# Kernel optimization log

Hardware: AMD Instinct MI355X
Metric: run time of the kernel (lower is better)

The kernel has to match this reference:

```python
import jax, jax.numpy as jnp
import numpy as np

N = 50000      # nodes
DEG = 32       # avg degree
E = N * DEG + N  # edges incl. self loops
IN_DIM = 512
H = 4          # heads
D = 128        # hidden per head
SLOPE = 0.2


def setup_inputs() -> dict:
    key = jax.random.key(0)
    ks = jax.random.split(key, 12)
    features = jax.random.normal(ks[0], (N, IN_DIM), dtype=jnp.float32)
    src_r = jax.random.randint(ks[1], (N * DEG,), 0, N)
    dst_r = jax.random.randint(ks[2], (N * DEG,), 0, N)
    loop = jnp.arange(N)
    src = jnp.concatenate([src_r, loop]).astype(jnp.int32)
    dst = jnp.concatenate([dst_r, loop]).astype(jnp.int32)
    ids = jax.random.randint(ks[3], (16,), 0, N)
    s0 = 1.0 / np.sqrt(IN_DIM)
    s1 = 1.0 / np.sqrt(H * D)
    fc_w0 = jax.random.normal(ks[4], (IN_DIM, H * D), dtype=jnp.float32) * s0
    attn_l0 = jax.random.normal(ks[5], (H, D), dtype=jnp.float32) * s1
    attn_r0 = jax.random.normal(ks[6], (H, D), dtype=jnp.float32) * s1
    bias0 = jnp.zeros((H * D,), dtype=jnp.float32)
    fc_w1 = jax.random.normal(ks[7], (H * D, H * D), dtype=jnp.float32) * s1
    attn_l1 = jax.random.normal(ks[8], (H, D), dtype=jnp.float32) * s1
    attn_r1 = jax.random.normal(ks[9], (H, D), dtype=jnp.float32) * s1
    bias1 = jnp.zeros((H * D,), dtype=jnp.float32)
    return dict(features=features, fc_w0=fc_w0, attn_l0=attn_l0, attn_r0=attn_r0,
                bias0=bias0, fc_w1=fc_w1, attn_l1=attn_l1, attn_r1=attn_r1,
                bias1=bias1, src=src, dst=dst, ids=ids)


def gat_layer(h, fc_w, attn_l, attn_r, bias, src, dst, residual):
    ft = (h @ fc_w).reshape(N, H, D)                     # [N,H,D]
    el = jnp.sum(ft * attn_l, axis=-1)                   # [N,H]
    er = jnp.sum(ft * attn_r, axis=-1)                   # [N,H]
    e = jax.nn.leaky_relu(el[src] + er[dst], SLOPE)      # [E,H]
    # edge softmax over incoming edges of each dst node (self-loops guarantee coverage)
    emax = jax.ops.segment_max(e, dst, num_segments=N)   # [N,H]
    ee = jnp.exp(e - emax[dst])
    esum = jax.ops.segment_sum(ee, dst, num_segments=N)  # [N,H]
    alpha = ee / esum[dst]                               # [E,H]
    out = jax.ops.segment_sum(alpha[:, :, None] * ft[src], dst, num_segments=N)  # [N,H,D]
    if residual:
        out = out + h.reshape(N, H, D)                   # res_fc is Identity (in == H*D)
    out = out + bias.reshape(1, H, D)
    out = jax.nn.elu(out)
    return out.reshape(N, H * D)


def reference(features, fc_w0, attn_l0, attn_r0, bias0, fc_w1, attn_l1, attn_r1,
              bias1, src, dst, ids):
    h = gat_layer(features, fc_w0, attn_l0, attn_r0, bias0, src, dst, residual=False)
    h = gat_layer(h, fc_w1, attn_l1, attn_r1, bias1, src, dst, residual=True)
    h = jnp.tanh(h)
    return h[ids]  # [B, H*D] gather per id2node lookup
```

## Files before the change

kernel.cpp:

```cpp
#include <hip/hip_runtime.h>
#include <hip/hip_bf16.h>

typedef short bf16x8 __attribute__((ext_vector_type(8)));
typedef float f32x4 __attribute__((ext_vector_type(4)));

#define HD 512
#define KDIM 512
#define NHEAD 4
#define DHEAD 128
#define C1CAP 1024
#define C2CAP 16384
#define E1CAP 2048
#define E2CAP 32768

__global__ void detect_k(const unsigned short* __restrict__ feat, int* __restrict__ flagp) {
    __shared__ int cs;
    if (threadIdx.x == 0) cs = 0;
    __syncthreads();
    int c = 0;
    for (int k = 0; k < 16; ++k) {
        unsigned short u = feat[2 * (threadIdx.x + k * 256)];
        int e = (u >> 7) & 0xFF;
        if (e >= 96 && e <= 140) c++;
    }
    atomicAdd(&cs, c);
    __syncthreads();
    if (threadIdx.x == 0) *flagp = (cs > 2048) ? 1 : 0;
}

__global__ __launch_bounds__(256) void prep_k(
    const void* __restrict__ W0, const void* __restrict__ W1,
    __hip_bfloat16* __restrict__ Wt0, __hip_bfloat16* __restrict__ Wt1,
    const void* p0, const void* p1, const void* p2,
    const void* p3, const void* p4, const void* p5,
    float* __restrict__ smallc,
    const int* __restrict__ ids, int B,
    int* __restrict__ mapId, unsigned* __restrict__ bmId,
    const int* __restrict__ flagp) {
    const int isbf = *flagp;
    const int b = blockIdx.x;
    const int t = threadIdx.x;
    if (b < 2048) {
        const void* W = (b < 1024) ? W0 : W1;
        __hip_bfloat16* Wt = (b < 1024) ? Wt0 : Wt1;
        int idx = ((b < 1024) ? b : b - 1024) * 256 + t;
        int i = idx >> 9;
        int j = idx & 511;
        float v = isbf ? __bfloat162float(((const __hip_bfloat16*)W)[idx])
                       : ((const float*)W)[idx];
        Wt[j * 512 + i] = __float2bfloat16(v);
    } else if (b < 2054) {
        int which = b - 2048;
        const void* p;
        switch (which) {
            case 0: p = p0; break;
            case 1: p = p1; break;
            case 2: p = p2; break;
            case 3: p = p3; break;
            case 4: p = p4; break;
            default: p = p5; break;
        }
#pragma unroll
        for (int r = 0; r < 2; ++r) {
            int e = t + r * 256;
            float v = isbf ? __bfloat162float(((const __hip_bfloat16*)p)[e])
                           : ((const float*)p)[e];
            smallc[which * 512 + e] = v;
        }
    } else {
        if (t < B) {
            int n = ids[t];
            mapId[n] = t;
            atomicOr(&bmId[n >> 5], 1u << (n & 31));
        }
    }
}

__global__ __launch_bounds__(256) void scan_k(
    const int* __restrict__ dst, int E,
    const unsigned* __restrict__ bm,
    unsigned long long* __restrict__ masks) {
    const int gid = blockIdx.x * 256 + threadIdx.x;
    const bool inb = (4 * gid < E);
    int4 d4 = {0, 0, 0, 0};
    if (inb) d4 = ((const int4*)dst)[gid];
    const int dv[4] = {d4.x, d4.y, d4.z, d4.w};
    unsigned long long m[4];
#pragma unroll
    for (int k = 0; k < 4; ++k) {
        int d = dv[k];
        bool hit = inb && ((bm[d >> 5] >> (d & 31)) & 1u);
        m[k] = __ballot(hit);
    }
    const int w = gid >> 6, lane = gid & 63;
    if (lane < 4) {
        unsigned long long v = (lane == 0) ? m[0] : (lane == 1) ? m[1]
                             : (lane == 2) ? m[2] : m[3];
        masks[(size_t)w * 4 + lane] = v;
    }
}

__global__ __launch_bounds__(256) void emit_k(
    const unsigned long long* __restrict__ masks, int nmask,
    const int* __restrict__ src, const int* __restrict__ dst,
    const int* __restrict__ mapd,
    int2* __restrict__ elist, int* __restrict__ ecnt, int cap,
    int* __restrict__ mapm, int* __restrict__ Flist,
    int* __restrict__ nF, int fcap, unsigned* __restrict__ bmOut) {
    int j = blockIdx.x * 256 + threadIdx.x;
    if (j >= nmask) return;
    unsigned long long m = masks[j];
    if (!m) return;
    const int w = j >> 2, k = j & 3;
    while (m) {
        int l = __ffsll((long long)m) - 1;
        m &= m - 1;
        int e = w * 256 + l * 4 + k;
        int s = src[e], d = dst[e];
        int p = atomicAdd(ecnt, 1);
        if (p < cap) { int2 v; v.x = s; v.y = mapd[d]; elist[p] = v; }
        if (atomicCAS(&mapm[s], -1, -2) == -1) {
            int q = atomicAdd(nF, 1);
            if (q < fcap) { Flist[q] = s; mapm[s] = q; }
            else mapm[s] = 0;
            if (bmOut) atomicOr(&bmOut[s >> 5], 1u << (s & 31));
        }
    }
}

__global__ __launch_bounds__(1024) void csr_k(
    const int2* __restrict__ E1, const int* __restrict__ nE1p,
    const int2* __restrict__ E2, const int* __restrict__ nE2p,
    const int* __restrict__ map1, const int* __restrict__ map2,
    int* __restrict__ off1, int* __restrict__ off2,
    int* __restrict__ b1, int* __restrict__ b2) {
    __shared__ int cnt[1024];
    __shared__ int scn[1024];
    __shared__ int cur[1024];
    __shared__ int c1[16];
    __shared__ int o1cur[16];
    const int t = threadIdx.x;
    int n1 = *nE1p; if (n1 > E1CAP) n1 = E1CAP;
    int n2 = *nE2p; if (n2 > E2CAP) n2 = E2CAP;
    cnt[t] = 0;
    if (t < 16) c1[t] = 0;
    __syncthreads();
    for (int i = t; i < n2; i += 1024) atomicAdd(&cnt[E2[i].y], 1);
    for (int i = t; i < n1; i += 1024) atomicAdd(&c1[E1[i].y], 1);
    __syncthreads();
    int v = cnt[t];
    scn[t] = v;
    __syncthreads();
    for (int off = 1; off < 1024; off <<= 1) {
        int x = (t >= off) ? scn[t - off] : 0;
        __syncthreads();
        scn[t] += x;
        __syncthreads();
    }
    int ex = scn[t] - v;
    off2[t] = ex;
    cur[t] = ex;
    if (t == 1023) off2[1024] = scn[1023];
    if (t == 0) {
        int a = 0;
        for (int i = 0; i < 16; ++i) { off1[i] = a; o1cur[i] = a; a += c1[i]; }
        off1[16] = a;
    }
    __syncthreads();
    for (int i = t; i < n2; i += 1024) {
        int p = atomicAdd(&cur[E2[i].y], 1);
        int r = map2[E2[i].x]; if (r < 0) r = 0;
        b2[p] = r;
    }
    for (int i = t; i < n1; i += 1024) {
        int p = atomicAdd(&o1cur[E1[i].y], 1);
        int r = map1[E1[i].x]; if (r < 0) r = 0;
        b1[p] = r;
    }
}

__global__ __launch_bounds__(256) void gatherA_k(const void* __restrict__ feat,
                                                 const int* __restrict__ F2list,
                                                 const int* __restrict__ nF2,
                                                 __hip_bfloat16* __restrict__ Ac,
                                                 const int* __restrict__ flagp) {
    int cnt = *nF2; if (cnt > C2CAP) cnt = C2CAP;
    const int isbf = *flagp;
    const int t = threadIdx.x;
    for (int b = blockIdx.x; b < cnt; b += gridDim.x) {
        int row = F2list[b];
        __hip_bfloat162 v;
        if (isbf) {
            v = *(const __hip_bfloat162*)&((const __hip_bfloat16*)feat)[(size_t)row * KDIM + t * 2];
        } else {
            const float2 f = *(const float2*)&((const float*)feat)[(size_t)row * KDIM + t * 2];
            v.x = __float2bfloat16(f.x);
            v.y = __float2bfloat16(f.y);
        }
        *(__hip_bfloat162*)&Ac[(size_t)b * KDIM + t * 2] = v;
    }
}

__global__ __launch_bounds__(256) void gemm_c(
    const __hip_bfloat16* __restrict__ A,
    const __hip_bfloat16* __restrict__ Bt,
    __hip_bfloat16* __restrict__ C,
    const int* __restrict__ countp) {
    const int cntv = *countp;
    const int m0 = blockIdx.y * 128;
    if (m0 >= cntv) return;
    __shared__ alignas(16) __hip_bfloat16 As[128][40];
    __shared__ alignas(16) __hip_bfloat16 Bs[128][40];
    const int t = threadIdx.x;
    const int n0 = blockIdx.x * 128;
    const int lane = t & 63, wave = t >> 6;
    const int wm = (wave >> 1) * 64, wn = (wave & 1) * 64;
    const int fr = lane & 15, fk = (lane >> 4) * 8;
    const int r0 = t >> 2;
    const int c0 = (t & 3) * 8;

    int arow[2];
#pragma unroll
    for (int r = 0; r < 2; ++r) {
        int rr = m0 + r * 64 + r0;
        if (rr >= cntv) rr = cntv - 1;
        arow[r] = rr;
    }

    f32x4 acc[4][4];
#pragma unroll
    for (int i = 0; i < 4; ++i)
#pragma unroll
        for (int j = 0; j < 4; ++j)
#pragma unroll
            for (int r = 0; r < 4; ++r) acc[i][j][r] = 0.f;

    for (int kt = 0; kt < KDIM; kt += 32) {
#pragma unroll
        for (int r = 0; r < 2; ++r) {
            int row = r * 64 + r0;
            uint4 va = *(const uint4*)&A[(size_t)arow[r] * KDIM + kt + c0];
            *(uint4*)&As[row][c0] = va;
            uint4 vb = *(const uint4*)&Bt[(size_t)(n0 + row) * KDIM + kt + c0];
            *(uint4*)&Bs[row][c0] = vb;
        }
        __syncthreads();
        bf16x8 af[4], bfr[4];
#pragma unroll
        for (int i = 0; i < 4; ++i) af[i]  = *(const bf16x8*)&As[wm + i * 16 + fr][fk];
#pragma unroll
        for (int j = 0; j < 4; ++j) bfr[j] = *(const bf16x8*)&Bs[wn + j * 16 + fr][fk];
#pragma unroll
        for (int i = 0; i < 4; ++i)
#pragma unroll
            for (int j = 0; j < 4; ++j)
                acc[i][j] = __builtin_amdgcn_mfma_f32_16x16x32_bf16(af[i], bfr[j], acc[i][j], 0, 0, 0);
        __syncthreads();
    }

    const int cr = (lane >> 4) * 4;
    const int cc = lane & 15;
#pragma unroll
    for (int i = 0; i < 4; ++i)
#pragma unroll
        for (int j = 0; j < 4; ++j)
#pragma unroll
            for (int rg = 0; rg < 4; ++rg) {
                int m = m0 + wm + i * 16 + cr + rg;
                int n = n0 + wn + j * 16 + cc;
                C[(size_t)m * HD + n] = __float2bfloat16(acc[i][j][rg]);
            }
}

__global__ __launch_bounds__(256) void elc_k(const __hip_bfloat16* __restrict__ ft,
                                             const float* __restrict__ attn_l,
                                             const float* __restrict__ attn_r,
                                             const int* __restrict__ countp,
                                             float* __restrict__ el, float* __restrict__ er) {
    int cnt = *countp; if (cnt > C2CAP) cnt = C2CAP;
    const int h = threadIdx.x >> 6, lane = threadIdx.x & 63;
    const float2 al = *(const float2*)&attn_l[h * DHEAD + lane * 2];
    const float2 ar = *(const float2*)&attn_r[h * DHEAD + lane * 2];
    for (int b = blockIdx.x; b < cnt; b += gridDim.x) {
        const __hip_bfloat162 f = *(const __hip_bfloat162*)&ft[(size_t)b * HD + h * DHEAD + lane * 2];
        float fx = __bfloat162float(f.x), fy = __bfloat162float(f.y);
        float pl = fx * al.x + fy * al.y;
        float pr = fx * ar.x + fy * ar.y;
        for (int off = 32; off; off >>= 1) {
            pl += __shfl_xor(pl, off, 64);
            pr += __shfl_xor(pr, off, 64);
        }
        if (lane == 0) {
            el[b * NHEAD + h] = pl;
            er[b * NHEAD + h] = pr;
        }
    }
}

__global__ __launch_bounds__(256) void agg1_k(
    const int* __restrict__ off2, const int* __restrict__ b2,
    const int* __restrict__ F1list, const int* __restrict__ map2,
    const int* __restrict__ nF1,
    const float* __restrict__ el, const float* __restrict__ er,
    const __hip_bfloat16* __restrict__ ftc,
    const float* __restrict__ bias,
    __hip_bfloat16* __restrict__ outc) {
    int b = blockIdx.x;
    if (b >= *nF1) return;
    int n = F1list[b];
    int h = threadIdx.x >> 6, lane = threadIdx.x & 63;
    int rn = map2[n]; if (rn < 0) rn = 0;
    float ern = er[rn * NHEAD + h];
    int beg = off2[b], end = off2[b + 1];
    float m = -3.0e38f, l = 0.f, a0 = 0.f, a1 = 0.f;
    for (int i = beg; i < end; ++i) {
        int r2 = b2[i];
        float e = el[r2 * NHEAD + h] + ern;
        e = (e >= 0.f) ? e : 0.2f * e;
        float mn = fmaxf(m, e);
        float sc = __expf(m - mn);
        float w  = __expf(e - mn);
        const __hip_bfloat162 f = *(const __hip_bfloat162*)&ftc[(size_t)r2 * HD + h * DHEAD + lane * 2];
        l  = l * sc + w;
        a0 = a0 * sc + w * __bfloat162float(f.x);
        a1 = a1 * sc + w * __bfloat162float(f.y);
        m = mn;
    }
    float inv = (l > 0.f) ? 1.0f / l : 0.f;
    float o0 = a0 * inv, o1 = a1 * inv;
    const float2 bb = *(const float2*)&bias[h * DHEAD + lane * 2];
    o0 += bb.x;
    o1 += bb.y;
    o0 = (o0 > 0.f) ? o0 : expm1f(o0);
    o1 = (o1 > 0.f) ? o1 : expm1f(o1);
    __hip_bfloat162 o2;
    o2.x = __float2bfloat16(o0);
    o2.y = __float2bfloat16(o1);
    *(__hip_bfloat162*)&outc[(size_t)b * HD + h * DHEAD + lane * 2] = o2;
}

__global__ __launch_bounds__(256) void agg2_k(
    const int* __restrict__ off1, const int* __restrict__ b1,
    const int* __restrict__ ids, const int* __restrict__ mapId,
    const int* __restrict__ map1,
    const float* __restrict__ el, const float* __restrict__ er,
    const __hip_bfloat16* __restrict__ ftc,
    const __hip_bfloat16* __restrict__ resc,
    const float* __restrict__ bias,
    void* __restrict__ out, const int* __restrict__ flagp) {
    int b = blockIdx.x;
    int n = ids[b];
    int slot = mapId[n]; if (slot < 0) slot = 0;
    int h = threadIdx.x >> 6, lane = threadIdx.x & 63;
    int rn = map1[n]; if (rn < 0) rn = 0;
    float ern = er[rn * NHEAD + h];
    int beg = off1[slot], end = off1[slot + 1];
    float m = -3.0e38f, l = 0.f, a0 = 0.f, a1 = 0.f;
    for (int i = beg; i < end; ++i) {
        int r1 = b1[i];
        float e = el[r1 * NHEAD + h] + ern;
        e = (e >= 0.f) ? e : 0.2f * e;
        float mn = fmaxf(m, e);
        float sc = __expf(m - mn);
        float w  = __expf(e - mn);
        const __hip_bfloat162 f = *(const __hip_bfloat162*)&ftc[(size_t)r1 * HD + h * DHEAD + lane * 2];
        l  = l * sc + w;
        a0 = a0 * sc + w * __bfloat162float(f.x);
        a1 = a1 * sc + w * __bfloat162float(f.y);
        m = mn;
    }
    float inv = (l > 0.f) ? 1.0f / l : 0.f;
    float o0 = a0 * inv, o1 = a1 * inv;
    const __hip_bfloat162 r2v = *(const __hip_bfloat162*)&resc[(size_t)rn * HD + h * DHEAD + lane * 2];
    o0 += __bfloat162float(r2v.x);
    o1 += __bfloat162float(r2v.y);
    const float2 bb = *(const float2*)&bias[h * DHEAD + lane * 2];
    o0 += bb.x;
    o1 += bb.y;
    o0 = (o0 > 0.f) ? o0 : expm1f(o0);
    o1 = (o1 > 0.f) ? o1 : expm1f(o1);
    o0 = tanhf(o0);
    o1 = tanhf(o1);
    size_t oi = (size_t)b * HD + h * DHEAD + lane * 2;
    if (*flagp) {
        __hip_bfloat162 o2;
        o2.x = __float2bfloat16(o0);
        o2.y = __float2bfloat16(o1);
        *(__hip_bfloat162*)&((__hip_bfloat16*)out)[oi] = o2;
    } else {
        float2 o2; o2.x = o0; o2.y = o1;
        *(float2*)&((float*)out)[oi] = o2;
    }
}

extern "C" void kernel_launch(void* const* d_in, const int* in_sizes, int n_in,
                              void* d_out, int out_size, void* d_ws, size_t ws_size,
                              hipStream_t stream) {
    const void* features = d_in[0];
    const void* fc_w0    = d_in[1];
    const void* attn_l0  = d_in[2];
    const void* attn_r0  = d_in[3];
    const void* bias0    = d_in[4];
    const void* fc_w1    = d_in[5];
    const void* attn_l1  = d_in[6];
    const void* attn_r1  = d_in[7];
    const void* bias1    = d_in[8];
    const int* src = (const int*)d_in[9];
    const int* dst = (const int*)d_in[10];
    const int* ids = (const int*)d_in[11];

    const int N = in_sizes[0] / KDIM;
    const int E = in_sizes[9];
    const int B = in_sizes[11];
    const int words = (N + 31) / 32;

    const int nblk_scan = (E + 1023) / 1024;
    const int nwaves    = nblk_scan * 4;
    const int nmask     = nwaves * 4;

    char* w = (char*)d_ws;
    auto alloc = [&](size_t bytes) {
        void* p = (void*)w;
        w += (bytes + 255) & ~(size_t)255;
        return p;
    };
    __hip_bfloat16* Wt0 = (__hip_bfloat16*)alloc(512 * 512 * 2);
    __hip_bfloat16* Wt1 = (__hip_bfloat16*)alloc(512 * 512 * 2);
    float* smallc = (float*)alloc(6 * 512 * 4);
    int* maps    = (int*)alloc((size_t)3 * N * 4);
    int* mapId = maps;
    int* map1  = maps + N;
    int* map2  = maps + 2 * N;
    unsigned long long* masks = (unsigned long long*)alloc((size_t)nmask * 8);
    int2* E1l  = (int2*)alloc((size_t)E1CAP * 8);
    int2* E2l  = (int2*)alloc((size_t)E2CAP * 8);
    int* F1list = (int*)alloc(C1CAP * 4);
    int* F2list = (int*)alloc(C2CAP * 4);
    const int zwords = 8 + 2 * words;
    int* zmem   = (int*)alloc((size_t)zwords * 4);
    int* counters = zmem;
    unsigned* bmId = (unsigned*)(zmem + 8);
    unsigned* bm1  = bmId + words;
    int* off1 = (int*)alloc(17 * 4);
    int* off2 = (int*)alloc(1025 * 4);
    int* b1   = (int*)alloc(E1CAP * 4);
    int* b2   = (int*)alloc(E2CAP * 4);
    __hip_bfloat16* Ac   = (__hip_bfloat16*)alloc((size_t)C2CAP * KDIM * 2);
    __hip_bfloat16* ft0c = (__hip_bfloat16*)alloc((size_t)C2CAP * HD * 2);
    float* el0 = (float*)alloc((size_t)C2CAP * NHEAD * 4);
    float* er0 = (float*)alloc((size_t)C2CAP * NHEAD * 4);
    __hip_bfloat16* h1c  = (__hip_bfloat16*)alloc((size_t)C1CAP * HD * 2);
    __hip_bfloat16* ft1c = (__hip_bfloat16*)alloc((size_t)C1CAP * HD * 2);
    float* el1 = (float*)alloc((size_t)C1CAP * NHEAD * 4);
    float* er1 = (float*)alloc((size_t)C1CAP * NHEAD * 4);

    int* nE1  = counters + 0;
    int* nE2  = counters + 1;
    int* nF1  = counters + 2;
    int* nF2  = counters + 3;
    int* flag = counters + 4;

    hipMemsetAsync(maps, 0xFF, (size_t)3 * N * 4, stream);
    hipMemsetAsync(zmem, 0, (size_t)zwords * 4, stream);

    detect_k<<<1, 256, 0, stream>>>((const unsigned short*)features, flag);
    prep_k<<<2055, 256, 0, stream>>>(fc_w0, fc_w1, Wt0, Wt1,
                                     attn_l0, attn_r0, bias0, attn_l1, attn_r1, bias1,
                                     smallc, ids, B, mapId, bmId, flag);
    float* al0c = smallc + 0 * 512;
    float* ar0c = smallc + 1 * 512;
    float* b0c  = smallc + 2 * 512;
    float* al1c = smallc + 3 * 512;
    float* ar1c = smallc + 4 * 512;
    float* b1c  = smallc + 5 * 512;

    scan_k<<<nblk_scan, 256, 0, stream>>>(dst, E, bmId, masks);
    emit_k<<<(nmask + 255) / 256, 256, 0, stream>>>(masks, nmask, src, dst, mapId,
                                                    E1l, nE1, E1CAP,
                                                    map1, F1list, nF1, C1CAP, bm1);
    scan_k<<<nblk_scan, 256, 0, stream>>>(dst, E, bm1, masks);
    emit_k<<<(nmask + 255) / 256, 256, 0, stream>>>(masks, nmask, src, dst, map1,
                                                    E2l, nE2, E2CAP,
                                                    map2, F2list, nF2, C2CAP, nullptr);

    csr_k<<<1, 1024, 0, stream>>>(E1l, nE1, E2l, nE2, map1, map2, off1, off2, b1, b2);

    gatherA_k<<<512, 256, 0, stream>>>(features, F2list, nF2, Ac, flag);
    gemm_c<<<dim3(HD / 128, C2CAP / 128), 256, 0, stream>>>(Ac, Wt0, ft0c, nF2);
    elc_k<<<512, 256, 0, stream>>>(ft0c, al0c, ar0c, nF2, el0, er0);
    agg1_k<<<C1CAP, 256, 0, stream>>>(off2, b2, F1list, map2, nF1,
                                      el0, er0, ft0c, b0c, h1c);

    gemm_c<<<dim3(HD / 128, C1CAP / 128), 256, 0, stream>>>(h1c, Wt1, ft1c, nF1);
    elc_k<<<512, 256, 0, stream>>>(ft1c, al1c, ar1c, nF1, el1, er1);
    agg2_k<<<B, 256, 0, stream>>>(off1, b1, ids, mapId, map1,
                                  el1, er1, ft1c, h1c, b1c,
                                  d_out, flag);
}
```

Before: 374.2 us.

## Fuse pipeline into two persistent kernels with software grid barriers

Replaces the chain of about a dozen small kernel launches with two persistent 512-block kernels that move from phase to phase through a global atomic-counter barrier. The BFS frontier scan and emit passes merge into one pass that buffers edges and frontier nodes in shared memory and reserves global slots in bulk, and it also counts CSR degrees as it goes. The aim is to remove launch gaps and the masks round trip. The cost is that the spin barrier assumes all 512 blocks are resident at once, which is not guaranteed without a cooperative launch, and the GEMM and aggregation phases now run at a fixed grid size.

Result: slower. 1.024 ms (+173.7%).

```diff
diff --git a/kernel.cpp b/kernel.cpp
--- a/kernel.cpp
+++ b/kernel.cpp
@@ -12,207 +12,103 @@
 #define C2CAP 16384
 #define E1CAP 2048
 #define E2CAP 32768
-
-__global__ void detect_k(const unsigned short* __restrict__ feat, int* __restrict__ flagp) {
-    __shared__ int cs;
-    if (threadIdx.x == 0) cs = 0;
-    __syncthreads();
+#define GA 512
+
+__device__ __forceinline__ void gbar(int* cnt, int& gen) {
+    __syncthreads();
+    if (threadIdx.x == 0) {
+        __threadfence();
+        atomicAdd(cnt, 1);
+        gen += GA;
+        while (__hip_atomic_load(cnt, __ATOMIC_ACQUIRE, __HIP_MEMORY_SCOPE_AGENT) < gen)
+            __builtin_amdgcn_s_sleep(2);
+    }
+    __syncthreads();
+}
+
+__device__ int detect_bf16(const unsigned short* f) {
     int c = 0;
-    for (int k = 0; k < 16; ++k) {
-        unsigned short u = feat[2 * (threadIdx.x + k * 256)];
+#pragma unroll
+    for (int k = 0; k < 4; ++k) {
+        unsigned short u = f[2 * (threadIdx.x + k * 256)];
         int e = (u >> 7) & 0xFF;
-        if (e >= 96 && e <= 140) c++;
-    }
-    atomicAdd(&cs, c);
-    __syncthreads();
-    if (threadIdx.x == 0) *flagp = (cs > 2048) ? 1 : 0;
-}
-
-__global__ __launch_bounds__(256) void prep_k(
-    const void* __restrict__ W0, const void* __restrict__ W1,
-    __hip_bfloat16* __restrict__ Wt0, __hip_bfloat16* __restrict__ Wt1,
-    const void* p0, const void* p1, const void* p2,
-    const void* p3, const void* p4, const void* p5,
-    float* __restrict__ smallc,
-    const int* __restrict__ ids, int B,
-    int* __restrict__ mapId, unsigned* __restrict__ bmId,
-    const int* __restrict__ flagp) {
-    const int isbf = *flagp;
-    const int b = blockIdx.x;
+        c += (e >= 96 && e <= 140) ? 1 : 0;
+    }
+#pragma unroll
+    for (int off = 32; off; off >>= 1) c += __shfl_xor(c, off, 64);
+    __shared__ int s_c;
+    if (threadIdx.x == 0) s_c = 0;
+    __syncthreads();
+    if ((threadIdx.x & 63) == 0) atomicAdd(&s_c, c);
+    __syncthreads();
+    return s_c > 512;
+}
+
+__device__ void bfs_pass(const int* __restrict__ src, const int* __restrict__ dst, int E,
+                         const unsigned* __restrict__ bmIn, const int* __restrict__ mapd,
+                         int2* __restrict__ elist, int* ecnt, int ecap,
+                         int* __restrict__ cntArr,
+                         int* __restrict__ mapm, int* __restrict__ Flist, int* nFr, int fcap,
+                         unsigned* bmOut) {
+    __shared__ int2 eBuf[256];
+    __shared__ int fBuf[256];
+    __shared__ int eCnt_s, fCnt_s, eBase_s, fBase_s;
     const int t = threadIdx.x;
-    if (b < 2048) {
-        const void* W = (b < 1024) ? W0 : W1;
-        __hip_bfloat16* Wt = (b < 1024) ? Wt0 : Wt1;
-        int idx = ((b < 1024) ? b : b - 1024) * 256 + t;
-        int i = idx >> 9;
-        int j = idx & 511;
-        float v = isbf ? __bfloat162float(((const __hip_bfloat16*)W)[idx])
-                       : ((const float*)W)[idx];
-        Wt[j * 512 + i] = __float2bfloat16(v);
-    } else if (b < 2054) {
-        int which = b - 2048;
-        const void* p;
-        switch (which) {
-            case 0: p = p0; break;
-            case 1: p = p1; break;
-            case 2: p = p2; break;
-            case 3: p = p3; break;
-            case 4: p = p4; break;
-            default: p = p5; break;
-        }
-#pragma unroll
-        for (int r = 0; r < 2; ++r) {
-            int e = t + r * 256;
-            float v = isbf ? __bfloat162float(((const __hip_bfloat16*)p)[e])
-                           : ((const float*)p)[e];
-            smallc[which * 512 + e] = v;
-        }
-    } else {
-        if (t < B) {
-            int n = ids[t];
-            mapId[n] = t;
-            atomicOr(&bmId[n >> 5], 1u << (n & 31));
-        }
-    }
-}
-
-__global__ __launch_bounds__(256) void scan_k(
-    const int* __restrict__ dst, int E,
-    const unsigned* __restrict__ bm,
-    unsigned long long* __restrict__ masks) {
-    const int gid = blockIdx.x * 256 + threadIdx.x;
-    const bool inb = (4 * gid < E);
-    int4 d4 = {0, 0, 0, 0};
-    if (inb) d4 = ((const int4*)dst)[gid];
-    const int dv[4] = {d4.x, d4.y, d4.z, d4.w};
-    unsigned long long m[4];
-#pragma unroll
-    for (int k = 0; k < 4; ++k) {
-        int d = dv[k];
-        bool hit = inb && ((bm[d >> 5] >> (d & 31)) & 1u);
-        m[k] = __ballot(hit);
-    }
-    const int w = gid >> 6, lane = gid & 63;
-    if (lane < 4) {
-        unsigned long long v = (lane == 0) ? m[0] : (lane == 1) ? m[1]
-                             : (lane == 2) ? m[2] : m[3];
-        masks[(size_t)w * 4 + lane] = v;
-    }
-}
-
-__global__ __launch_bounds__(256) void emit_k(
-    const unsigned long long* __restrict__ masks, int nmask,
-    const int* __restrict__ src, const int* __restrict__ dst,
-    const int* __restrict__ mapd,
-    int2* __restrict__ elist, int* __restrict__ ecnt, int cap,
-    int* __restrict__ mapm, int* __restrict__ Flist,
-    int* __restrict__ nF, int fcap, unsigned* __restrict__ bmOut) {
-    int j = blockIdx.x * 256 + threadIdx.x;
-    if (j >= nmask) return;
-    unsigned long long m = masks[j];
-    if (!m) return;
-    const int w = j >> 2, k = j & 3;
-    while (m) {
-        int l = __ffsll((long long)m) - 1;
-        m &= m - 1;
-        int e = w * 256 + l * 4 + k;
-        int s = src[e], d = dst[e];
-        int p = atomicAdd(ecnt, 1);
-        if (p < cap) { int2 v; v.x = s; v.y = mapd[d]; elist[p] = v; }
-        if (atomicCAS(&mapm[s], -1, -2) == -1) {
-            int q = atomicAdd(nF, 1);
-            if (q < fcap) { Flist[q] = s; mapm[s] = q; }
-            else mapm[s] = 0;
-            if (bmOut) atomicOr(&bmOut[s >> 5], 1u << (s & 31));
-        }
-    }
-}
-
-__global__ __launch_bounds__(1024) void csr_k(
-    const int2* __restrict__ E1, const int* __restrict__ nE1p,
-    const int2* __restrict__ E2, const int* __restrict__ nE2p,
-    const int* __restrict__ map1, const int* __restrict__ map2,
-    int* __restrict__ off1, int* __restrict__ off2,
-    int* __restrict__ b1, int* __restrict__ b2) {
-    __shared__ int cnt[1024];
-    __shared__ int scn[1024];
-    __shared__ int cur[1024];
-    __shared__ int c1[16];
-    __shared__ int o1cur[16];
+    if (t == 0) { eCnt_s = 0; fCnt_s = 0; }
+    __syncthreads();
+    const int nq = E >> 2;
+    for (int gid = blockIdx.x * 256 + t; gid < nq; gid += GA * 256) {
+        const int4 d4 = ((const int4*)dst)[gid];
+        const int dv[4] = {d4.x, d4.y, d4.z, d4.w};
+#pragma unroll
+        for (int k = 0; k < 4; ++k) {
+            const int d = dv[k];
+            if ((bmIn[d >> 5] >> (d & 31)) & 1u) {
+                const int e = 4 * gid + k;
+                int2 v; v.x = src[e]; v.y = mapd[d];
+                int p = atomicAdd(&eCnt_s, 1);
+                if (p < 256) eBuf[p] = v;
+                else {
+                    int q = atomicAdd(ecnt, 1);
+                    if (q < ecap) { elist[q] = v; atomicAdd(&cntArr[v.y], 1); }
+                }
+                const int s = v.x;
+                if (atomicCAS(&mapm[s], -1, -2) == -1) {
+                    int q = atomicAdd(&fCnt_s, 1);
+                    if (q < 256) fBuf[q] = s;
+                    else {
+                        int g2 = atomicAdd(nFr, 1);
+                        if (g2 < fcap) { Flist[g2] = s; mapm[s] = g2; }
+                        else mapm[s] = 0;
+                    }
+                    if (bmOut) atomicOr(&bmOut[s >> 5], 1u << (s & 31));
+                }
+            }
+        }
+    }
+    __syncthreads();
+    const int ne = (eCnt_s < 256) ? eCnt_s : 256;
+    const int nf = (fCnt_s < 256) ? fCnt_s : 256;
+    if (t == 0 && ne) eBase_s = atomicAdd(ecnt, ne);
+    if (t == 64 && nf) fBase_s = atomicAdd(nFr, nf);
+    __syncthreads();
+    for (int i = t; i < ne; i += 256) {
+        int p = eBase_s + i;
+        if (p < ecap) { int2 v = eBuf[i]; elist[p] = v; atomicAdd(&cntArr[v.y], 1); }
+    }
+    for (int i = t; i < nf; i += 256) {
+        int q = fBase_s + i; int s = fBuf[i];
+        if (q < fcap) { Flist[q] = s; mapm[s] = q; }
+        else mapm[s] = 0;
+    }
+}
+
+__device__ void gemm_tile(const __hip_bfloat16* __restrict__ A,
+                          const __hip_bfloat16* __restrict__ Bt,
+                          __hip_bfloat16* __restrict__ C,
+                          int cntv, int m0, int n0,
+                          __hip_bfloat16 (*As)[40], __hip_bfloat16 (*Bs)[40]) {
     const int t = threadIdx.x;
-    int n1 = *nE1p; if (n1 > E1CAP) n1 = E1CAP;
-    int n2 = *nE2p; if (n2 > E2CAP) n2 = E2CAP;
-    cnt[t] = 0;
-    if (t < 16) c1[t] = 0;
-    __syncthreads();
-    for (int i = t; i < n2; i += 1024) atomicAdd(&cnt[E2[i].y], 1);
-    for (int i = t; i < n1; i += 1024) atomicAdd(&c1[E1[i].y], 1);
-    __syncthreads();
-    int v = cnt[t];
-    scn[t] = v;
-    __syncthreads();
-    for (int off = 1; off < 1024; off <<= 1) {
-        int x = (t >= off) ? scn[t - off] : 0;
-        __syncthreads();
-        scn[t] += x;
-        __syncthreads();
-    }
-    int ex = scn[t] - v;
-    off2[t] = ex;
-    cur[t] = ex;
-    if (t == 1023) off2[1024] = scn[1023];
-    if (t == 0) {
-        int a = 0;
-        for (int i = 0; i < 16; ++i) { off1[i] = a; o1cur[i] = a; a += c1[i]; }
-        off1[16] = a;
-    }
-    __syncthreads();
-    for (int i = t; i < n2; i += 1024) {
-        int p = atomicAdd(&cur[E2[i].y], 1);
-        int r = map2[E2[i].x]; if (r < 0) r = 0;
-        b2[p] = r;
-    }
-    for (int i = t; i < n1; i += 1024) {
-        int p = atomicAdd(&o1cur[E1[i].y], 1);
-        int r = map1[E1[i].x]; if (r < 0) r = 0;
-        b1[p] = r;
-    }
-}
-
-__global__ __launch_bounds__(256) void gatherA_k(const void* __restrict__ feat,
-                                                 const int* __restrict__ F2list,
-                                                 const int* __restrict__ nF2,
-                                                 __hip_bfloat16* __restrict__ Ac,
-                                                 const int* __restrict__ flagp) {
-    int cnt = *nF2; if (cnt > C2CAP) cnt = C2CAP;
-    const int isbf = *flagp;
-    const int t = threadIdx.x;
-    for (int b = blockIdx.x; b < cnt; b += gridDim.x) {
-        int row = F2list[b];
-        __hip_bfloat162 v;
-        if (isbf) {
-            v = *(const __hip_bfloat162*)&((const __hip_bfloat16*)feat)[(size_t)row * KDIM + t * 2];
-        } else {
-            const float2 f = *(const float2*)&((const float*)feat)[(size_t)row * KDIM + t * 2];
-            v.x = __float2bfloat16(f.x);
-            v.y = __float2bfloat16(f.y);
-        }
-        *(__hip_bfloat162*)&Ac[(size_t)b * KDIM + t * 2] = v;
-    }
-}
-
-__global__ __launch_bounds__(256) void gemm_c(
-    const __hip_bfloat16* __restrict__ A,
-    const __hip_bfloat16* __restrict__ Bt,
-    __hip_bfloat16* __restrict__ C,
-    const int* __restrict__ countp) {
-    const int cntv = *countp;
-    const int m0 = blockIdx.y * 128;
-    if (m0 >= cntv) return;
-    __shared__ alignas(16) __hip_bfloat16 As[128][40];
-    __shared__ alignas(16) __hip_bfloat16 Bs[128][40];
-    const int t = threadIdx.x;
-    const int n0 = blockIdx.x * 128;
     const int lane = t & 63, wave = t >> 6;
     const int wm = (wave >> 1) * 64, wn = (wave & 1) * 64;
     const int fr = lane & 15, fk = (lane >> 4) * 8;
@@ -272,16 +168,13 @@
             }
 }
 
-__global__ __launch_bounds__(256) void elc_k(const __hip_bfloat16* __restrict__ ft,
-                                             const float* __restrict__ attn_l,
-                                             const float* __restrict__ attn_r,
-                                             const int* __restrict__ countp,
-                                             float* __restrict__ el, float* __restrict__ er) {
-    int cnt = *countp; if (cnt > C2CAP) cnt = C2CAP;
+__device__ void elc_phase(const __hip_bfloat16* __restrict__ ft,
+                          const float* __restrict__ al_, const float* __restrict__ ar_,
+                          int cnt, float* __restrict__ el, float* __restrict__ er) {
     const int h = threadIdx.x >> 6, lane = threadIdx.x & 63;
-    const float2 al = *(const float2*)&attn_l[h * DHEAD + lane * 2];
-    const float2 ar = *(const float2*)&attn_r[h * DHEAD + lane * 2];
-    for (int b = blockIdx.x; b < cnt; b += gridDim.x) {
+    const float2 al = *(const float2*)&al_[h * DHEAD + lane * 2];
+    const float2 ar = *(const float2*)&ar_[h * DHEAD + lane * 2];
+    for (int b = blockIdx.x; b < cnt; b += GA) {
         const __hip_bfloat162 f = *(const __hip_bfloat162*)&ft[(size_t)b * HD + h * DHEAD + lane * 2];
         float fx = __bfloat162float(f.x), fy = __bfloat162float(f.y);
         float pl = fx * al.x + fy * al.y;
@@ -297,99 +190,246 @@
     }
 }
 
-__global__ __launch_bounds__(256) void agg1_k(
-    const int* __restrict__ off2, const int* __restrict__ b2,
-    const int* __restrict__ F1list, const int* __restrict__ map2,
-    const int* __restrict__ nF1,
-    const float* __restrict__ el, const float* __restrict__ er,
-    const __hip_bfloat16* __restrict__ ftc,
-    const float* __restrict__ bias,
-    __hip_bfloat16* __restrict__ outc) {
-    int b = blockIdx.x;
-    if (b >= *nF1) return;
-    int n = F1list[b];
-    int h = threadIdx.x >> 6, lane = threadIdx.x & 63;
-    int rn = map2[n]; if (rn < 0) rn = 0;
-    float ern = er[rn * NHEAD + h];
-    int beg = off2[b], end = off2[b + 1];
-    float m = -3.0e38f, l = 0.f, a0 = 0.f, a1 = 0.f;
-    for (int i = beg; i < end; ++i) {
-        int r2 = b2[i];
-        float e = el[r2 * NHEAD + h] + ern;
-        e = (e >= 0.f) ? e : 0.2f * e;
-        float mn = fmaxf(m, e);
-        float sc = __expf(m - mn);
-        float w  = __expf(e - mn);
-        const __hip_bfloat162 f = *(const __hip_bfloat162*)&ftc[(size_t)r2 * HD + h * DHEAD + lane * 2];
-        l  = l * sc + w;
-        a0 = a0 * sc + w * __bfloat162float(f.x);
-        a1 = a1 * sc + w * __bfloat162float(f.y);
-        m = mn;
-    }
-    float inv = (l > 0.f) ? 1.0f / l : 0.f;
-    float o0 = a0 * inv, o1 = a1 * inv;
-    const float2 bb = *(const float2*)&bias[h * DHEAD + lane * 2];
-    o0 += bb.x;
-    o1 += bb.y;
-    o0 = (o0 > 0.f) ? o0 : expm1f(o0);
-    o1 = (o1 > 0.f) ? o1 : expm1f(o1);
-    __hip_bfloat162 o2;
-    o2.x = __float2bfloat16(o0);
-    o2.y = __float2bfloat16(o1);
-    *(__hip_bfloat162*)&outc[(size_t)b * HD + h * DHEAD + lane * 2] = o2;
-}
-
-__global__ __launch_bounds__(256) void agg2_k(
-    const int* __restrict__ off1, const int* __restrict__ b1,
-    const int* __restrict__ ids, const int* __restrict__ mapId,
-    const int* __restrict__ map1,
-    const float* __restrict__ el, const float* __restrict__ er,
-    const __hip_bfloat16* __restrict__ ftc,
-    const __hip_bfloat16* __restrict__ resc,
-    const float* __restrict__ bias,
-    void* __restrict__ out, const int* __restrict__ flagp) {
-    int b = blockIdx.x;
-    int n = ids[b];
-    int slot = mapId[n]; if (slot < 0) slot = 0;
-    int h = threadIdx.x >> 6, lane = threadIdx.x & 63;
-    int rn = map1[n]; if (rn < 0) rn = 0;
-    float ern = er[rn * NHEAD + h];
-    int beg = off1[slot], end = off1[slot + 1];
-    float m = -3.0e38f, l = 0.f, a0 = 0.f, a1 = 0.f;
-    for (int i = beg; i < end; ++i) {
-        int r1 = b1[i];
-        float e = el[r1 * NHEAD + h] + ern;
-        e = (e >= 0.f) ? e : 0.2f * e;
-        float mn = fmaxf(m, e);
-        float sc = __expf(m - mn);
-        float w  = __expf(e - mn);
-        const __hip_bfloat162 f = *(const __hip_bfloat162*)&ftc[(size_t)r1 * HD + h * DHEAD + lane * 2];
-        l  = l * sc + w;
-        a0 = a0 * sc + w * __bfloat162float(f.x);
-        a1 = a1 * sc + w * __bfloat162float(f.y);
-        m = mn;
-    }
-    float inv = (l > 0.f) ? 1.0f / l : 0.f;
-    float o0 = a0 * inv, o1 = a1 * inv;
-    const __hip_bfloat162 r2v = *(const __hip_bfloat162*)&resc[(size_t)rn * HD + h * DHEAD + lane * 2];
-    o0 += __bfloat162float(r2v.x);
-    o1 += __bfloat162float(r2v.y);
-    const float2 bb = *(const float2*)&bias[h * DHEAD + lane * 2];
-    o0 += bb.x;
-    o1 += bb.y;
-    o0 = (o0 > 0.f) ? o0 : expm1f(o0);
-    o1 = (o1 > 0.f) ? o1 : expm1f(o1);
-    o0 = tanhf(o0);
-    o1 = tanhf(o1);
-    size_t oi = (size_t)b * HD + h * DHEAD + lane * 2;
-    if (*flagp) {
-        __hip_bfloat162 o2;
-        o2.x = __float2bfloat16(o0);
-        o2.y = __float2bfloat16(o1);
-        *(__hip_bfloat162*)&((__hip_bfloat16*)out)[oi] = o2;
-    } else {
-        float2 o2; o2.x = o0; o2.y = o1;
-        *(float2*)&((float*)out)[oi] = o2;
+struct PrepArgs {
+    const void* features; const void* W0; const void* W1;
+    __hip_bfloat16* Wt0; __hip_bfloat16* Wt1;
+    const void* sp[6];
+    float* smallc;
+    const int* ids; int B;
+    const int* src; const int* dst; int E;
+    int* mapId; int* map1; int* map2;
+    unsigned* bmId; unsigned* bm1;
+    int2* E1l; int2* E2l; int* F1list; int* F2list;
+    int* counters;
+    int* cnt1; int* cnt2;
+    int* off1; int* off2; int* cur1; int* cur2;
+    int* b1; int* b2;
+    __hip_bfloat16* Ac;
+    int* bar;
+};
+
+__global__ __launch_bounds__(256, 2) void coopA(PrepArgs a) {
+    const int t = threadIdx.x;
+    int gen = 0;
+    const int isbf = detect_bf16((const unsigned short*)a.features);
+
+    for (int vb = blockIdx.x; vb < 2048; vb += GA) {
+        const void* W = (vb < 1024) ? a.W0 : a.W1;
+        __hip_bfloat16* Wt = (vb < 1024) ? a.Wt0 : a.Wt1;
+        int idx = (vb & 1023) * 256 + t;
+        int i = idx >> 9, j = idx & 511;
+        float v = isbf ? __bfloat162float(((const __hip_bfloat16*)W)[idx])
+                       : ((const float*)W)[idx];
+        Wt[j * 512 + i] = __float2bfloat16(v);
+    }
+    if (blockIdx.x < 6) {
+        const void* p = a.sp[blockIdx.x];
+#pragma unroll
+        for (int r = 0; r < 2; ++r) {
+            int e = t + r * 256;
+            float v = isbf ? __bfloat162float(((const __hip_bfloat16*)p)[e])
+                           : ((const float*)p)[e];
+            a.smallc[blockIdx.x * 512 + e] = v;
+        }
+    }
+    if (blockIdx.x == 6 && t < a.B) {
+        int n = a.ids[t];
+        a.mapId[n] = t;
+        atomicOr(&a.bmId[n >> 5], 1u << (n & 31));
+    }
+    gbar(a.bar, gen);
+
+    bfs_pass(a.src, a.dst, a.E, a.bmId, a.mapId, a.E1l, a.counters + 0, E1CAP,
+             a.cnt1, a.map1, a.F1list, a.counters + 2, C1CAP, a.bm1);
+    gbar(a.bar, gen);
+
+    bfs_pass(a.src, a.dst, a.E, a.bm1, a.map1, a.E2l, a.counters + 1, E2CAP,
+             a.cnt2, a.map2, a.F2list, a.counters + 3, C2CAP, nullptr);
+    gbar(a.bar, gen);
+
+    if (blockIdx.x == 0) {
+        __shared__ int sc[256];
+        int c0 = a.cnt2[t * 4 + 0], c1 = a.cnt2[t * 4 + 1];
+        int c2 = a.cnt2[t * 4 + 2], c3 = a.cnt2[t * 4 + 3];
+        int tsum = c0 + c1 + c2 + c3;
+        sc[t] = tsum;
+        __syncthreads();
+        for (int off = 1; off < 256; off <<= 1) {
+            int x = (t >= off) ? sc[t - off] : 0;
+            __syncthreads();
+            sc[t] += x;
+            __syncthreads();
+        }
+        int run = sc[t] - tsum;
+        int b4 = t * 4;
+        a.off2[b4 + 0] = run; a.cur2[b4 + 0] = run; run += c0;
+        a.off2[b4 + 1] = run; a.cur2[b4 + 1] = run; run += c1;
+        a.off2[b4 + 2] = run; a.cur2[b4 + 2] = run; run += c2;
+        a.off2[b4 + 3] = run; a.cur2[b4 + 3] = run; run += c3;
+        if (t == 255) a.off2[1024] = run;
+        if (t == 0) {
+            int acc = 0;
+            for (int i = 0; i < 16; ++i) { a.off1[i] = acc; a.cur1[i] = acc; acc += a.cnt1[i]; }
+            a.off1[16] = acc;
+        }
+    }
+    {
+        int cntF2 = a.counters[3]; if (cntF2 > C2CAP) cntF2 = C2CAP;
+        for (int b = blockIdx.x; b < cntF2; b += GA) {
+            int row = a.F2list[b];
+            __hip_bfloat162 v;
+            if (isbf) {
+                v = *(const __hip_bfloat162*)&((const __hip_bfloat16*)a.features)[(size_t)row * KDIM + t * 2];
+            } else {
+                const float2 f = *(const float2*)&((const float*)a.features)[(size_t)row * KDIM + t * 2];
+                v.x = __float2bfloat16(f.x);
+                v.y = __float2bfloat16(f.y);
+            }
+            *(__hip_bfloat162*)&a.Ac[(size_t)b * KDIM + t * 2] = v;
+        }
+    }
+    gbar(a.bar, gen);
+
+    {
+        int n2 = a.counters[1]; if (n2 > E2CAP) n2 = E2CAP;
+        for (int i = blockIdx.x * 256 + t; i < n2; i += GA * 256) {
+            int2 v = a.E2l[i];
+            int p = atomicAdd(&a.cur2[v.y], 1);
+            int r = a.map2[v.x]; if (r < 0) r = 0;
+            a.b2[p] = r;
+        }
+        int n1 = a.counters[0]; if (n1 > E1CAP) n1 = E1CAP;
+        for (int i = blockIdx.x * 256 + t; i < n1; i += GA * 256) {
+            int2 v = a.E1l[i];
+            int p = atomicAdd(&a.cur1[v.y], 1);
+            int r = a.map1[v.x]; if (r < 0) r = 0;
+            a.b1[p] = r;
+        }
+    }
+}
+
+struct ComputeArgs {
+    const void* features;
+    const __hip_bfloat16* Ac; const __hip_bfloat16* Wt0; const __hip_bfloat16* Wt1;
+    __hip_bfloat16* ft0c; __hip_bfloat16* ft1c; __hip_bfloat16* h1c;
+    const float* smallc;
+    float* el0; float* er0; float* el1; float* er1;
+    const int* counters;
+    const int* off1; const int* off2; const int* b1; const int* b2;
+    const int* ids; const int* mapId; const int* map1; const int* map2;
+    const int* F1list;
+    void* out; int B;
+    int* bar;
+};
+
+__global__ __launch_bounds__(256, 2) void coopB(ComputeArgs a) {
+    __shared__ alignas(16) __hip_bfloat16 As[128][40];
+    __shared__ alignas(16) __hip_bfloat16 Bs[128][40];
+    const int t = threadIdx.x;
+    int gen = 0;
+    const int isbf = detect_bf16((const unsigned short*)a.features);
+    int cnt2 = a.counters[3]; if (cnt2 > C2CAP) cnt2 = C2CAP;
+    int cnt1 = a.counters[2]; if (cnt1 > C1CAP) cnt1 = C1CAP;
+
+    {
+        int nt = ((cnt2 + 127) >> 7) * 4;
+        for (int tile = blockIdx.x; tile < nt; tile += GA)
+            gemm_tile(a.Ac, a.Wt0, a.ft0c, cnt2, (tile >> 2) * 128, (tile & 3) * 128, As, Bs);
+    }
+    gbar(a.bar, gen);
+
+    elc_phase(a.ft0c, a.smallc, a.smallc + 512, cnt2, a.el0, a.er0);
+    gbar(a.bar, gen);
+
+    {
+        const int h = t >> 6, lane = t & 63;
+        for (int b = blockIdx.x; b < cnt1; b += GA) {
+            int n = a.F1list[b];
+            int rn = a.map2[n]; if (rn < 0) rn = 0;
+            float ern = a.er0[rn * NHEAD + h];
+            int beg = a.off2[b], end = a.off2[b + 1];
+            float m = -3.0e38f, l = 0.f, a0 = 0.f, a1 = 0.f;
+            for (int i = beg; i < end; ++i) {
+                int r2 = a.b2[i];
+                float e = a.el0[r2 * NHEAD + h] + ern;
+                e = (e >= 0.f) ? e : 0.2f * e;
+                float mn = fmaxf(m, e);
+                float sc = __expf(m - mn);
+                float w  = __expf(e - mn);
+                const __hip_bfloat162 f = *(const __hip_bfloat162*)&a.ft0c[(size_t)r2 * HD + h * DHEAD + lane * 2];
+                l  = l * sc + w;
+                a0 = a0 * sc + w * __bfloat162float(f.x);
+                a1 = a1 * sc + w * __bfloat162float(f.y);
+                m = mn;
+            }
+            float inv = (l > 0.f) ? 1.0f / l : 0.f;
+            float o0 = a0 * inv, o1 = a1 * inv;
+            const float2 bb = *(const float2*)&a.smallc[1024 + h * DHEAD + lane * 2];
+            o0 += bb.x; o1 += bb.y;
+            o0 = (o0 > 0.f) ? o0 : expm1f(o0);
+            o1 = (o1 > 0.f) ? o1 : expm1f(o1);
+            __hip_bfloat162 o2;
+            o2.x = __float2bfloat16(o0);
+            o2.y = __float2bfloat16(o1);
+            *(__hip_bfloat162*)&a.h1c[(size_t)b * HD + h * DHEAD + lane * 2] = o2;
+        }
+    }
+    gbar(a.bar, gen);
+
+    {
+        int nt = ((cnt1 + 127) >> 7) * 4;
+        for (int tile = blockIdx.x; tile < nt; tile += GA)
+            gemm_tile(a.h1c, a.Wt1, a.ft1c, cnt1, (tile >> 2) * 128, (tile & 3) * 128, As, Bs);
+    }
+    gbar(a.bar, gen);
+
+    elc_phase(a.ft1c, a.smallc + 1536, a.smallc + 2048, cnt1, a.el1, a.er1);
+    gbar(a.bar, gen);
+
+    {
+        const int h = t >> 6, lane = t & 63;
+        for (int b = blockIdx.x; b < a.B; b += GA) {
+            int n = a.ids[b];
+            int slot = a.mapId[n]; if (slot < 0) slot = 0;
+            int rn = a.map1[n]; if (rn < 0) rn = 0;
+            float ern = a.er1[rn * NHEAD + h];
+            int beg = a.off1[slot], end = a.off1[slot + 1];
+            float m = -3.0e38f, l = 0.f, a0 = 0.f, a1 = 0.f;
+            for (int i = beg; i < end; ++i) {
+                int r1 = a.b1[i];
+                float e = a.el1[r1 * NHEAD + h] + ern;
+                e = (e >= 0.f) ? e : 0.2f * e;
+                float mn = fmaxf(m, e);
+                float sc = __expf(m - mn);
+                float w  = __expf(e - mn);
+                const __hip_bfloat162 f = *(const __hip_bfloat162*)&a.ft1c[(size_t)r1 * HD + h * DHEAD + lane * 2];
+                l  = l * sc + w;
+                a0 = a0 * sc + w * __bfloat162float(f.x);
+                a1 = a1 * sc + w * __bfloat162float(f.y);
+                m = mn;
+            }
+            float inv = (l > 0.f) ? 1.0f / l : 0.f;
+            float o0 = a0 * inv, o1 = a1 * inv;
+            const __hip_bfloat162 rv = *(const __hip_bfloat162*)&a.h1c[(size_t)rn * HD + h * DHEAD + lane * 2];
+            o0 += __bfloat162float(rv.x);
+            o1 += __bfloat162float(rv.y);
+            const float2 bb = *(const float2*)&a.smallc[2560 + h * DHEAD + lane * 2];
+            o0 += bb.x; o1 += bb.y;
+            o0 = (o0 > 0.f) ? o0 : expm1f(o0);
+            o1 = (o1 > 0.f) ? o1 : expm1f(o1);
+            o0 = tanhf(o0);
+            o1 = tanhf(o1);
+            size_t oi = (size_t)b * HD + h * DHEAD + lane * 2;
+            if (isbf) {
+                __hip_bfloat162 o2;
+                o2.x = __float2bfloat16(o0);
+                o2.y = __float2bfloat16(o1);
+                *(__hip_bfloat162*)&((__hip_bfloat16*)a.out)[oi] = o2;
+            } else {
+                float2 o2; o2.x = o0; o2.y = o1;
+                *(float2*)&((float*)a.out)[oi] = o2;
+            }
+        }
     }
 }
 
@@ -414,10 +454,6 @@
     const int B = in_sizes[11];
     const int words = (N + 31) / 32;
 
-    const int nblk_scan = (E + 1023) / 1024;
-    const int nwaves    = nblk_scan * 4;
-    const int nmask     = nwaves * 4;
-
     char* w = (char*)d_ws;
     auto alloc = [&](size_t bytes) {
         void* p = (void*)w;
@@ -427,22 +463,27 @@
     __hip_bfloat16* Wt0 = (__hip_bfloat16*)alloc(512 * 512 * 2);
     __hip_bfloat16* Wt1 = (__hip_bfloat16*)alloc(512 * 512 * 2);
     float* smallc = (float*)alloc(6 * 512 * 4);
-    int* maps    = (int*)alloc((size_t)3 * N * 4);
+    int* maps  = (int*)alloc((size_t)3 * N * 4);
     int* mapId = maps;
     int* map1  = maps + N;
     int* map2  = maps + 2 * N;
-    unsigned long long* masks = (unsigned long long*)alloc((size_t)nmask * 8);
     int2* E1l  = (int2*)alloc((size_t)E1CAP * 8);
     int2* E2l  = (int2*)alloc((size_t)E2CAP * 8);
     int* F1list = (int*)alloc(C1CAP * 4);
     int* F2list = (int*)alloc(C2CAP * 4);
-    const int zwords = 8 + 2 * words;
-    int* zmem   = (int*)alloc((size_t)zwords * 4);
+    const int zwords = 8 + 2 * words + 16 + 1024 + 32;
+    int* zmem = (int*)alloc((size_t)zwords * 4);
     int* counters = zmem;
     unsigned* bmId = (unsigned*)(zmem + 8);
     unsigned* bm1  = bmId + words;
+    int* cnt1 = (int*)(bm1 + words);
+    int* cnt2 = cnt1 + 16;
+    int* barA = cnt2 + 1024;
+    int* barB = barA + 16;
     int* off1 = (int*)alloc(17 * 4);
     int* off2 = (int*)alloc(1025 * 4);
+    int* cur1 = (int*)alloc(16 * 4);
+    int* cur2 = (int*)alloc(1024 * 4);
     int* b1   = (int*)alloc(E1CAP * 4);
     int* b2   = (int*)alloc(E2CAP * 4);
     __hip_bfloat16* Ac   = (__hip_bfloat16*)alloc((size_t)C2CAP * KDIM * 2);
@@ -454,46 +495,37 @@
     float* el1 = (float*)alloc((size_t)C1CAP * NHEAD * 4);
     float* er1 = (float*)alloc((size_t)C1CAP * NHEAD * 4);
 
-    int* nE1  = counters + 0;
-    int* nE2  = counters + 1;
-    int* nF1  = counters + 2;
-    int* nF2  = counters + 3;
-    int* flag = counters + 4;
-
     hipMemsetAsync(maps, 0xFF, (size_t)3 * N * 4, stream);
     hipMemsetAsync(zmem, 0, (size_t)zwords * 4, stream);
 
-    detect_k<<<1, 256, 0, stream>>>((const unsigned short*)features, flag);
-    prep_k<<<2055, 256, 0, stream>>>(fc_w0, fc_w1, Wt0, Wt1,
-                                     attn_l0, attn_r0, bias0, attn_l1, attn_r1, bias1,
-                                     smallc, ids, B, mapId, bmId, flag);
-    float* al0c = smallc + 0 * 512;
-    float* ar0c = smallc + 1 * 512;
-    float* b0c  = smallc + 2 * 512;
-    float* al1c = smallc + 3 * 512;
-    float* ar1c = smallc + 4 * 512;
-    float* b1c  = smallc + 5 * 512;
-
-    scan_k<<<nblk_scan, 256, 0, stream>>>(dst, E, bmId, masks);
-    emit_k<<<(nmask + 255) / 256, 256, 0, stream>>>(masks, nmask, src, dst, mapId,
-                                                    E1l, nE1, E1CAP,
-                                                    map1, F1list, nF1, C1CAP, bm1);
-    scan_k<<<nblk_scan, 256, 0, stream>>>(dst, E, bm1, masks);
-    emit_k<<<(nmask + 255) / 256, 256, 0, stream>>>(masks, nmask, src, dst, map1,
-                                                    E2l, nE2, E2CAP,
-                                                    map2, F2list, nF2, C2CAP, nullptr);
-
-    csr_k<<<1, 1024, 0, stream>>>(E1l, nE1, E2l, nE2, map1, map2, off1, off2, b1, b2);
-
-    gatherA_k<<<512, 256, 0, stream>>>(features, F2list, nF2, Ac, flag);
-    gemm_c<<<dim3(HD / 128, C2CAP / 128), 256, 0, stream>>>(Ac, Wt0, ft0c, nF2);
-    elc_k<<<512, 256, 0, stream>>>(ft0c, al0c, ar0c, nF2, el0, er0);
-    agg1_k<<<C1CAP, 256, 0, stream>>>(off2, b2, F1list, map2, nF1,
-                                      el0, er0, ft0c, b0c, h1c);
-
-    gemm_c<<<dim3(HD / 128, C1CAP / 128), 256, 0, stream>>>(h1c, Wt1, ft1c, nF1);
-    elc_k<<<512, 256, 0, stream>>>(ft1c, al1c, ar1c, nF1, el1, er1);
-    agg2_k<<<B, 256, 0, stream>>>(off1, b1, ids, mapId, map1,
-                                  el1, er1, ft1c, h1c, b1c,
-                                  d_out, flag);
-}
+    PrepArgs pa;
+    pa.features = features; pa.W0 = fc_w0; pa.W1 = fc_w1;
+    pa.Wt0 = Wt0; pa.Wt1 = Wt1;
+    pa.sp[0] = attn_l0; pa.sp[1] = attn_r0; pa.sp[2] = bias0;
+    pa.sp[3] = attn_l1; pa.sp[4] = attn_r1; pa.sp[5] = bias1;
+    pa.smallc = smallc;
+    pa.ids = ids; pa.B = B;
+    pa.src = src; pa.dst = dst; pa.E = E;
+    pa.mapId = mapId; pa.map1 = map1; pa.map2 = map2;
+    pa.bmId = bmId; pa.bm1 = bm1;
+    pa.E1l = E1l; pa.E2l = E2l; pa.F1list = F1list; pa.F2list = F2list;
+    pa.counters = counters; pa.cnt1 = cnt1; pa.cnt2 = cnt2;
+    pa.off1 = off1; pa.off2 = off2; pa.cur1 = cur1; pa.cur2 = cur2;
+    pa.b1 = b1; pa.b2 = b2;
+    pa.Ac = Ac; pa.bar = barA;
+    coopA<<<GA, 256, 0, stream>>>(pa);
+
+    ComputeArgs ca;
+    ca.features = features;
+    ca.Ac = Ac; ca.Wt0 = Wt0; ca.Wt1 = Wt1;
+    ca.ft0c = ft0c; ca.ft1c = ft1c; ca.h1c = h1c;
+    ca.smallc = smallc;
+    ca.el0 = el0; ca.er0 = er0; ca.el1 = el1; ca.er1 = er1;
+    ca.counters = counters;
+    ca.off1 = off1; ca.off2 = off2; ca.b1 = b1; ca.b2 = b2;
+    ca.ids = ids; ca.mapId = mapId; ca.map1 = map1; ca.map2 = map2;
+    ca.F1list = F1list;
+    ca.out = d_out; ca.B = B;
+    ca.bar = barB;
+    coopB<<<GA, 256, 0, stream>>>(ca);
+}
```
